# Optimization experiments

Measured on AMD Instinct MI355X. Metric: run time of the kernel, lower is better.

Reference implementation:

```python
import jax, jax.numpy as jnp
import numpy as np

EPS = 1e-5
B, S, D = 4, 2048, 128
BALL_SCALE = 0.05  # keeps points inside the unit Poincare ball for c=1


def setup_inputs() -> dict:
    key = jax.random.key(0)
    kq, kk, kv = jax.random.split(key, 3)
    q = jax.random.normal(kq, (B, S, D), dtype=jnp.float32) * BALL_SCALE
    k = jax.random.normal(kk, (B, S, D), dtype=jnp.float32) * BALL_SCALE
    v_tangent = jax.random.normal(kv, (B, S, D), dtype=jnp.float32)
    c = jnp.asarray(1.0, dtype=jnp.float32)
    beta = jnp.asarray(0.0, dtype=jnp.float32)            # nn.Parameter init 0.0
    attention_bias = jnp.asarray(0.0, dtype=jnp.float32)  # nn.Parameter init 0.0
    return {"q": q, "k": k, "v_tangent": v_tangent, "c": c,
            "beta": beta, "attention_bias": attention_bias}


def reference(q, k, v_tangent, c, beta, attention_bias):
    sqrt_c = jnp.sqrt(c)

    # --- pairwise Poincare distance (all fp32, as in the torch autocast block) ---
    x_norm_sq = jnp.sum(q * q, axis=-1, keepdims=True)            # (B,S,1)
    y_norm_sq = jnp.sum(k * k, axis=-1, keepdims=True)            # (B,S,1)
    xy_dot = jnp.einsum('bsd,btd->bst', q, k)                     # (B,S,S)
    y_norm_sq_t = jnp.swapaxes(y_norm_sq, -2, -1)                 # (B,1,S)
    diff_norm_sq = x_norm_sq - 2.0 * xy_dot + y_norm_sq_t         # ||x-y||^2, (B,S,S)
    denom = (1.0 - c * x_norm_sq) * (1.0 - c * y_norm_sq_t)       # (B,S,S)
    arg = 1.0 + 2.0 * c * diff_norm_sq / jnp.maximum(denom, EPS)
    dist = jnp.arccosh(jnp.maximum(arg, 1.0 + EPS)) / sqrt_c      # (B,S,S)

    # --- attention ---
    beta_positive = jax.nn.softplus(beta)
    attention_scores = -beta_positive * dist - attention_bias
    attention_weights = jax.nn.softmax(attention_scores, axis=-1)  # (B,S,S)
    output_tangent = jnp.einsum('bst,btd->bsd', attention_weights, v_tangent)

    # --- exp map at origin ---
    v_norm = jnp.maximum(
        jnp.sqrt(jnp.sum(output_tangent * output_tangent, axis=-1, keepdims=True)), EPS)
    output_hyperbolic = (jnp.tanh(sqrt_c * v_norm) / sqrt_c) * (output_tangent / v_norm)

    return output_hyperbolic, attention_weights
```

## Files before the change

### kernel.cpp

```cpp
#include <hip/hip_runtime.h>
#include <math.h>

#define B_ 4
#define S_ 2048
#define D_ 128
#define EPSF 1e-5f
#define BN 128
#define BN2 64
#define PSB 272

typedef __attribute__((ext_vector_type(8))) short short8;
typedef __attribute__((ext_vector_type(4))) float f32x4;

static __device__ __forceinline__ unsigned short f2bf(float f) {
    unsigned u = __float_as_uint(f);
    return (unsigned short)((u + 0x7fffu + ((u >> 16) & 1u)) >> 16);
}

static __device__ __forceinline__ void gload_lds16(const void* g, void* l) {
    __builtin_amdgcn_global_load_lds((const __attribute__((address_space(1))) unsigned*)g,
                                     (__attribute__((address_space(3))) unsigned*)l, 16, 0, 0);
}


__global__ __launch_bounds__(256) void convqk_kernel(const float* __restrict__ q,
                                                     const float* __restrict__ k,
                                                     const float* __restrict__ cp,
                                                     float* __restrict__ qn, float* __restrict__ kn,
                                                     float* __restrict__ lws,
                                                     float2* __restrict__ qng, float2* __restrict__ kng,
                                                     unsigned* __restrict__ Qb, unsigned* __restrict__ Kb) {
    int row = blockIdx.x * 4 + (threadIdx.x >> 6);
    int lane = threadIdx.x & 63;
    const int NR = B_ * S_;
    const float cc = cp[0];
    bool isQ = row < NR;
    int r = isQ ? row : row - NR;
    float2 v = ((const float2*)(isQ ? q : k))[(size_t)r * 64 + lane];
    unsigned pk = (unsigned)f2bf(v.x) | ((unsigned)f2bf(v.y) << 16);
    float nrm = v.x * v.x + v.y * v.y;
#pragma unroll
    for (int m = 1; m <= 32; m <<= 1) nrm += __shfl_xor(nrm, m, 64);
    if (isQ) {
        Qb[(size_t)r * 64 + lane] = pk;
        if (lane == 0) {
            qn[r] = nrm;
            qng[r] = make_float2(nrm, 2.f * cc * __builtin_amdgcn_rcpf(1.f - cc * nrm));
        }
        if (lane == 1) lws[r] = 0.f;
    } else {
        int c = lane >> 2;
        int cs = c ^ (r & 7);
        Kb[(size_t)r * 64 + cs * 4 + (lane & 3)] = pk;
        if (lane == 0) {
            kn[r] = nrm;
            kng[r] = make_float2(nrm, __builtin_amdgcn_rcpf(1.f - cc * nrm));
        }
    }
}

__global__ __launch_bounds__(256) void convv_kernel(const float* __restrict__ v, uint4* __restrict__ Vtb) {
    __shared__ unsigned short Vs[128 * 132];
    int b = blockIdx.x >> 4;
    int t = blockIdx.x & 15;
    int tid = threadIdx.x;
    const float* src = v + ((size_t)b * S_ + t * 128) * D_;
    int d4 = tid & 31, key0 = tid >> 5;
#pragma unroll
    for (int it = 0; it < 16; ++it) {
        int key = key0 + it * 8;
        float4 f = *(const float4*)(src + (size_t)key * D_ + d4 * 4);
        unsigned short* dst = &Vs[key * 132 + d4 * 4];
        dst[0] = f2bf(f.x); dst[1] = f2bf(f.y); dst[2] = f2bf(f.z); dst[3] = f2bf(f.w);
    }
    __syncthreads();
    uint4* tile = Vtb + (size_t)blockIdx.x * (128 * 16);
    int d = tid & 127;
    int cl = tid >> 7;
#pragma unroll
    for (int it = 0; it < 8; ++it) {
        int c = cl + it * 2;
        int kb = c * 8;
        unsigned short e0 = Vs[(kb + 0) * 132 + d], e1 = Vs[(kb + 1) * 132 + d];
        unsigned short e2 = Vs[(kb + 2) * 132 + d], e3 = Vs[(kb + 3) * 132 + d];
        unsigned short e4 = Vs[(kb + 4) * 132 + d], e5 = Vs[(kb + 5) * 132 + d];
        unsigned short e6 = Vs[(kb + 6) * 132 + d], e7 = Vs[(kb + 7) * 132 + d];
        uint4 o;
        o.x = (unsigned)e0 | ((unsigned)e1 << 16);
        o.y = (unsigned)e2 | ((unsigned)e3 << 16);
        o.z = (unsigned)e4 | ((unsigned)e5 << 16);
        o.w = (unsigned)e6 | ((unsigned)e7 << 16);
        tile[d * 16 + (c ^ (d & 7))] = o;
    }
}


__global__ __launch_bounds__(512, 2) void hattn3_kernel(
    const unsigned short* __restrict__ Qb, const char* __restrict__ Kb, const char* __restrict__ Vtb,
    const float2* __restrict__ qng, const float2* __restrict__ kng,
    const float* __restrict__ cp, const float* __restrict__ betap, const float* __restrict__ biasp,
    float* __restrict__ lws, float* __restrict__ Opart, uint4* __restrict__ Pws) {

    __shared__ __align__(1024) char smem[75648];
    char* PsB = smem + 65536;
    float* l_row = (float*)(smem + 75520);

    const int tid = threadIdx.x;
    const int lane = tid & 63, wave = tid >> 6;
    const int wm = wave & 1, wn = wave >> 1;
    const int lm = lane & 15, quad = lane >> 4;

    const int th = blockIdx.x & 1;
    const int b = (blockIdx.x >> 1) & 3;
    const int rb = blockIdx.x >> 3;
    const int s0 = rb * 32;
    const size_t bS = (size_t)b * S_;
    const int g0 = th * 16;

    const float beta = betap[0], bias = biasp[0];
    const float cc = cp[0];
    const float beta_pos = fmaxf(beta, 0.f) + log1pf(__expf(-fabsf(beta)));
    const float sqrt_c = sqrtf(cc);
    const float bneg = -beta_pos / sqrt_c;
    const float bias2 = -bias * 1.442695040888963f;
    const float onepe = 1.f + EPSF;

    const char* KbBase = Kb + bS * 256;
    const char* VtBase = Vtb + (size_t)b * 16 * 32768;

    {
        const char* ks = KbBase + (size_t)g0 * 16384;
        const char* vs = VtBase + (size_t)(g0 >> 1) * 32768 + (size_t)(g0 & 1) * 128;
#pragma unroll
        for (int j = 0; j < 2; ++j) {
            int m = tid + j * 512;
            gload_lds16(ks + m * 16, smem + m * 16);
            gload_lds16(vs + (m >> 3) * 256 + (m & 7) * 16, smem + 32768 + m * 16);
        }
        if (tid < 64) {
            float2 y = kng[bS + (size_t)g0 * 64 + tid];
            *(float2*)(smem + 74240 + tid * 8) = y;
        }
        if (tid >= 64 && tid < 96) {
            float2 x = qng[bS + s0 + (tid - 64)];
            *(float2*)(smem + 75264 + (tid - 64) * 8) = x;
        }
        if (tid >= 96 && tid < 128) l_row[tid - 96] = 0.f;
    }

    short8 aq[4];
    {
        const unsigned short* qrow = Qb + (bS + s0 + wm * 16 + lm) * D_;
#pragma unroll
        for (int ks = 0; ks < 4; ++ks)
            aq[ks] = *(const short8*)(qrow + ks * 32 + quad * 8);
    }

    f32x4 o0 = {0.f, 0.f, 0.f, 0.f}, o1 = {0.f, 0.f, 0.f, 0.f};
    float lacc[4] = {0.f, 0.f, 0.f, 0.f};

    __syncthreads();

    int p = 0;
    const int n0 = wn * 16 + lm;
    for (int it = 0; it < 16; ++it) {
        char* KsC = smem + p * 16384;
        char* VtC = smem + 32768 + p * 16384;
        const char* YGC = smem + 74240 + p * 512;

        float2 ygn;
        if (it < 15) {
            int g = g0 + it + 1;
            const char* ks = KbBase + (size_t)g * 16384;
            char* kd = smem + (p ^ 1) * 16384;
#pragma unroll
            for (int j = 0; j < 2; ++j) {
                int off = (tid + j * 512) * 16;
                gload_lds16(ks + off, kd + off);
            }
            if (tid < 64) ygn = kng[bS + (size_t)g * 64 + tid];
        }

        f32x4 acc = {0.f, 0.f, 0.f, 0.f};
#pragma unroll
        for (int ks = 0; ks < 4; ++ks) {
            int c = ks * 4 + quad;
            short8 bk = *(const short8*)(KsC + n0 * 256 + ((c ^ (n0 & 7)) * 16));
            acc = __builtin_amdgcn_mfma_f32_16x16x32_bf16(aq[ks], bk, acc, 0, 0, 0);
        }

        {
            float2 yg = *(const float2*)(YGC + n0 * 8);
#pragma unroll
            for (int r = 0; r < 4; ++r) {
                int row = wm * 16 + quad * 4 + r;
                float2 xr = *(const float2*)(smem + 75264 + row * 8);
                float diff = fmaf(-2.f, acc[r], xr.x + yg.x);
                float arg = fmaf(diff * yg.y, xr.y, 1.f);
                arg = fmaxf(arg, onepe);
                float w = arg + sqrtf(fmaf(arg, arg, -1.f));
                float pv = __builtin_amdgcn_exp2f(fmaf(bneg, __builtin_amdgcn_logf(w), bias2));
                *(unsigned short*)(PsB + row * PSB + n0 * 2) = f2bf(pv);
                lacc[r] += pv;
            }
        }
        __syncthreads();

        if (it < 15) {
            int g = g0 + it + 1;
            const char* vs = VtBase + (size_t)(g >> 1) * 32768 + (size_t)(g & 1) * 128;
            char* vd = smem + 32768 + (p ^ 1) * 16384;
#pragma unroll
            for (int j = 0; j < 2; ++j) {
                int m = tid + j * 512;
                gload_lds16(vs + (m >> 3) * 256 + (m & 7) * 16, vd + m * 16);
            }
            if (tid < 64) *(float2*)(smem + 74240 + (p ^ 1) * 512 + tid * 8) = ygn;
        }

        if (tid < 256) {
            int row = tid >> 3, ch = tid & 7;
            uint4 pv = *(const uint4*)(PsB + row * PSB + ch * 16);
            Pws[(((bS + s0 + row) * S_ + (size_t)(g0 + it) * 64) >> 3) + ch] = pv;
        }

#pragma unroll
        for (int ks2 = 0; ks2 < 2; ++ks2) {
            short8 ap = *(const short8*)(PsB + (wm * 16 + lm) * PSB + (ks2 * 32 + quad * 8) * 2);
            int d0 = wn * 32 + lm;
            int lo = ks2 * 4 + quad;
            short8 v0 = *(const short8*)(VtC + d0 * 128 + ((lo ^ (d0 & 7)) * 16));
            int d1 = d0 + 16;
            short8 v1 = *(const short8*)(VtC + d1 * 128 + ((lo ^ (d1 & 7)) * 16));
            o0 = __builtin_amdgcn_mfma_f32_16x16x32_bf16(ap, v0, o0, 0, 0, 0);
            o1 = __builtin_amdgcn_mfma_f32_16x16x32_bf16(ap, v1, o1, 0, 0, 0);
        }
        __syncthreads();
        p ^= 1;
    }

#pragma unroll
    for (int r = 0; r < 4; ++r) {
        float s = lacc[r];
#pragma unroll
        for (int m = 1; m <= 8; m <<= 1) s += __shfl_xor(s, m, 64);
        if (lm == 0) atomicAdd(&l_row[wm * 16 + quad * 4 + r], s);
    }
    __syncthreads();

    float* op = Opart + (size_t)th * (B_ * S_ * D_) + (bS + s0) * D_;
#pragma unroll
    for (int r = 0; r < 4; ++r) {
        int row = wm * 16 + quad * 4 + r;
        op[(size_t)row * D_ + wn * 32 + lm] = o0[r];
        op[(size_t)row * D_ + wn * 32 + 16 + lm] = o1[r];
    }
    if (tid < 32) atomicAdd(&lws[bS + s0 + tid], l_row[tid]);
}

__global__ __launch_bounds__(256) void hepi_kernel(const float* __restrict__ Opart,
                                                   const float* __restrict__ lws,
                                                   const float* __restrict__ cp,
                                                   float* __restrict__ hout) {
    int row = blockIdx.x * 4 + (threadIdx.x >> 6);
    int lane = threadIdx.x & 63;
    const float cc = cp[0];
    const float sqrt_c = sqrtf(cc);
    float2 a = ((const float2*)(Opart + (size_t)row * D_))[lane];
    float2 b = ((const float2*)(Opart + (size_t)(B_ * S_ * D_) + (size_t)row * D_))[lane];
    float linv = 1.f / lws[row];
    float x0 = (a.x + b.x) * linv;
    float x1 = (a.y + b.y) * linv;
    float np = x0 * x0 + x1 * x1;
#pragma unroll
    for (int m = 1; m <= 32; m <<= 1) np += __shfl_xor(np, m, 64);
    float vn = fmaxf(sqrtf(np), EPSF);
    float aa = sqrt_c * vn;
    float t = 1.f - 2.f / (__expf(2.f * aa) + 1.f);
    float sc = t / aa;
    float2 o = {x0 * sc, x1 * sc};
    ((float2*)(hout + (size_t)row * D_))[lane] = o;
}

__global__ __launch_bounds__(256) void wnorm2_kernel(const uint4* __restrict__ Pws,
                                                     const float* __restrict__ lws,
                                                     float* __restrict__ w) {
    size_t idx = (size_t)blockIdx.x * 256 + threadIdx.x;
    int row = (int)(idx >> 8);
    float linv = 1.f / lws[row];
    uint4 u = Pws[idx];
    float4 f0, f1;
    f0.x = __uint_as_float(u.x << 16) * linv;
    f0.y = __uint_as_float(u.x & 0xffff0000u) * linv;
    f0.z = __uint_as_float(u.y << 16) * linv;
    f0.w = __uint_as_float(u.y & 0xffff0000u) * linv;
    f1.x = __uint_as_float(u.z << 16) * linv;
    f1.y = __uint_as_float(u.z & 0xffff0000u) * linv;
    f1.z = __uint_as_float(u.w << 16) * linv;
    f1.w = __uint_as_float(u.w & 0xffff0000u) * linv;
    float4* out = (float4*)w + idx * 2;
    out[0] = f0;
    out[1] = f1;
}


__global__ __launch_bounds__(512, 2) void hattn_kernel(
    const unsigned short* __restrict__ Qb, const char* __restrict__ Kb, const char* __restrict__ Vtb,
    const float* __restrict__ qn, const float* __restrict__ kn,
    const float* __restrict__ cp, const float* __restrict__ betap, const float* __restrict__ biasp,
    float* __restrict__ lws, float* __restrict__ houtg, float* __restrict__ woutg) {

    __shared__ __align__(1024) char smem[75136];
    char* KsB = smem;
    char* VtB = smem + 32768;
    char* PsB = smem + 65536;
    float* kn_s  = (float*)(smem + 74240);
    float* qn_s  = (float*)(smem + 74752);
    float* l_row = (float*)(smem + 74880);
    float* nsq_s = (float*)(smem + 75008);

    const int tid = threadIdx.x;
    const int lane = tid & 63, wave = tid >> 6;
    const int wm = wave & 1, wn = wave >> 1;
    const int lm = lane & 15, quad = lane >> 4;

    int xcd = blockIdx.x & 7;
    int b = xcd >> 1;
    int rb = (blockIdx.x >> 3) * 2 + (xcd & 1);
    int s0 = rb * 32;
    const size_t bS = (size_t)b * S_;

    const float cc = cp[0], beta = betap[0], bias = biasp[0];
    const float beta_pos = fmaxf(beta, 0.f) + log1pf(__expf(-fabsf(beta)));
    const float sqrt_c = sqrtf(cc);
    const float inv_sqrt_c = 1.f / sqrt_c;

    if (tid < 32) {
        qn_s[tid] = qn[bS + s0 + tid];
        l_row[tid] = 0.f;
        nsq_s[tid] = 0.f;
    }

    short8 aq[4];
    {
        const unsigned short* qrow = Qb + (bS + s0 + wm * 16 + lm) * D_;
#pragma unroll
        for (int ks = 0; ks < 4; ++ks)
            aq[ks] = *(const short8*)(qrow + ks * 32 + quad * 8);
    }

    f32x4 o0 = {0.f, 0.f, 0.f, 0.f}, o1 = {0.f, 0.f, 0.f, 0.f};

    const char* KbBase = Kb + bS * 256;
    const char* VtBase = Vtb + (size_t)b * 16 * 32768;

    for (int t = 0; t < S_ / BN; ++t) {
        int t0 = t * BN;
        __syncthreads();
        {
            const uint4* ksrc = (const uint4*)(KbBase + (size_t)t0 * 256);
            const uint4* vsrc = (const uint4*)(VtBase + (size_t)t * 32768);
            uint4* kd = (uint4*)KsB;
            uint4* vd = (uint4*)VtB;
#pragma unroll
            for (int i = 0; i < 4; ++i) {
                kd[tid + i * 512] = ksrc[tid + i * 512];
                vd[tid + i * 512] = vsrc[tid + i * 512];
            }
            if (tid < BN) kn_s[tid] = kn[bS + t0 + tid];
        }
        __syncthreads();

        f32x4 acc0 = {0.f, 0.f, 0.f, 0.f}, acc1 = {0.f, 0.f, 0.f, 0.f};
#pragma unroll
        for (int ks = 0; ks < 4; ++ks) {
            int n0 = wn * 32 + lm;
            int c = ks * 4 + quad;
            short8 b0 = *(const short8*)(KsB + n0 * 256 + ((c ^ (n0 & 7)) * 16));
            int n1 = n0 + 16;
            short8 b1 = *(const short8*)(KsB + n1 * 256 + ((c ^ (n1 & 7)) * 16));
            acc0 = __builtin_amdgcn_mfma_f32_16x16x32_bf16(aq[ks], b0, acc0, 0, 0, 0);
            acc1 = __builtin_amdgcn_mfma_f32_16x16x32_bf16(aq[ks], b1, acc1, 0, 0, 0);
        }

        float lp[4];
#pragma unroll
        for (int r = 0; r < 4; ++r) {
            int row = wm * 16 + quad * 4 + r;
            float xn = qn_s[row];
            float fx = 1.f - cc * xn;
            float p0, p1;
#pragma unroll
            for (int nt = 0; nt < 2; ++nt) {
                int col = wn * 32 + nt * 16 + lm;
                float dot = (nt == 0) ? acc0[r] : acc1[r];
                float yn = kn_s[col];
                float diff = xn - 2.f * dot + yn;
                float den = fmaxf(fx * (1.f - cc * yn), EPSF);
                float arg = fmaf(2.f * cc * diff, __builtin_amdgcn_rcpf(den), 1.f);
                arg = fmaxf(arg, 1.f + EPSF);
                float dist = __logf(arg + sqrtf(arg * arg - 1.f)) * inv_sqrt_c;
                float p = __expf(fmaf(-beta_pos, dist, -bias));
                woutg[(bS + s0 + row) * S_ + t0 + col] = p;
                *(unsigned short*)(PsB + row * PSB + col * 2) = f2bf(p);
                if (nt == 0) p0 = p; else p1 = p;
            }
            lp[r] = p0 + p1;
        }
#pragma unroll
        for (int r = 0; r < 4; ++r) {
            float s = lp[r];
#pragma unroll
            for (int m = 1; m <= 8; m <<= 1) s += __shfl_xor(s, m, 64);
            if (lm == 0) atomicAdd(&l_row[wm * 16 + quad * 4 + r], s);
        }
        __syncthreads();

#pragma unroll
        for (int ks = 0; ks < 4; ++ks) {
            short8 ap = *(const short8*)(PsB + (wm * 16 + lm) * PSB + (ks * 32 + quad * 8) * 2);
            int d0 = wn * 32 + lm;
            int c = ks * 4 + quad;
            short8 v0 = *(const short8*)(VtB + d0 * 256 + ((c ^ (d0 & 7)) * 16));
            int d1 = d0 + 16;
            short8 v1 = *(const short8*)(VtB + d1 * 256 + ((c ^ (d1 & 7)) * 16));
            o0 = __builtin_amdgcn_mfma_f32_16x16x32_bf16(ap, v0, o0, 0, 0, 0);
            o1 = __builtin_amdgcn_mfma_f32_16x16x32_bf16(ap, v1, o1, 0, 0, 0);
        }
    }
    __syncthreads();

    float xs0[4], xs1[4];
#pragma unroll
    for (int r = 0; r < 4; ++r) {
        int row = wm * 16 + quad * 4 + r;
        float linv = __builtin_amdgcn_rcpf(l_row[row]);
        float x0 = o0[r] * linv, x1 = o1[r] * linv;
        xs0[r] = x0; xs1[r] = x1;
        float np = x0 * x0 + x1 * x1;
#pragma unroll
        for (int m = 1; m <= 8; m <<= 1) np += __shfl_xor(np, m, 64);
        if (lm == 0) atomicAdd(&nsq_s[row], np);
    }
    if (tid < 32) lws[bS + s0 + tid] = l_row[tid];
    __syncthreads();
#pragma unroll
    for (int r = 0; r < 4; ++r) {
        int row = wm * 16 + quad * 4 + r;
        float vn = fmaxf(sqrtf(nsq_s[row]), EPSF);
        float a = sqrt_c * vn;
        float th = 1.f - 2.f * __builtin_amdgcn_rcpf(__expf(2.f * a) + 1.f);
        float sc = th / a;
        houtg[(bS + s0 + row) * D_ + wn * 32 + lm] = xs0[r] * sc;
        houtg[(bS + s0 + row) * D_ + wn * 32 + 16 + lm] = xs1[r] * sc;
    }
}

__global__ __launch_bounds__(256) void wnorm_kernel(float* __restrict__ w,
                                                    const float* __restrict__ lws) {
    size_t idx = (size_t)blockIdx.x * 256 + threadIdx.x;
    int row = (int)(idx >> 9);
    float linv = 1.f / lws[row];
    float4* p = (float4*)w + idx;
    float4 v = *p;
    v.x *= linv; v.y *= linv; v.z *= linv; v.w *= linv;
    *p = v;
}


extern "C" void kernel_launch(void* const* d_in, const int* in_sizes, int n_in,
                              void* d_out, int out_size, void* d_ws, size_t ws_size,
                              hipStream_t stream) {
    const float* q    = (const float*)d_in[0];
    const float* k    = (const float*)d_in[1];
    const float* v    = (const float*)d_in[2];
    const float* c    = (const float*)d_in[3];
    const float* beta = (const float*)d_in[4];
    const float* ab   = (const float*)d_in[5];

    float* out  = (float*)d_out;
    float* hout = out;
    float* wout = out + (size_t)B_ * S_ * D_;

    float* qn  = (float*)d_ws;
    float* kn  = qn + B_ * S_;
    float* lws = kn + B_ * S_;
    char*  wsb = (char*)d_ws;
    const size_t QG_OFF = 98304;
    const size_t KG_OFF = QG_OFF + 65536;
    const size_t QB_OFF = KG_OFF + 65536;
    const size_t KB_OFF = QB_OFF + 2097152;
    const size_t VT_OFF = KB_OFF + 2097152;
    const size_t NEED1  = VT_OFF + 2097152;
    const size_t OP_OFF = NEED1;
    const size_t PW_OFF = OP_OFF + 2u * B_ * S_ * D_ * 4;
    const size_t NEED2  = PW_OFF + (size_t)B_ * S_ * S_ * 2;

    float2*  qng = (float2*)(wsb + QG_OFF);
    float2*  kng = (float2*)(wsb + KG_OFF);
    unsigned* Qb = (unsigned*)(wsb + QB_OFF);
    unsigned* Kb = (unsigned*)(wsb + KB_OFF);
    uint4*   Vtb = (uint4*)(wsb + VT_OFF);

    if (ws_size >= NEED2) {
        float* Opart = (float*)(wsb + OP_OFF);
        uint4* Pws   = (uint4*)(wsb + PW_OFF);
        convqk_kernel<<<4096, 256, 0, stream>>>(q, k, c, qn, kn, lws, qng, kng, Qb, Kb);
        convv_kernel<<<64, 256, 0, stream>>>(v, Vtb);
        hattn3_kernel<<<512, 512, 0, stream>>>((const unsigned short*)Qb, (const char*)Kb,
                                               (const char*)Vtb, qng, kng, c, beta, ab,
                                               lws, Opart, Pws);
        hepi_kernel<<<2048, 256, 0, stream>>>(Opart, lws, c, hout);
        wnorm2_kernel<<<8192, 256, 0, stream>>>(Pws, lws, wout);
    } else {
        convqk_kernel<<<4096, 256, 0, stream>>>(q, k, c, qn, kn, lws, qng, kng, Qb, Kb);
        convv_kernel<<<64, 256, 0, stream>>>(v, Vtb);
        hattn_kernel<<<256, 512, 0, stream>>>((const unsigned short*)Qb, (const char*)Kb,
                                              (const char*)Vtb, qn, kn, c, beta, ab,
                                              lws, hout, wout);
        wnorm_kernel<<<(B_ * S_ * S_ / 4) / 256, 256, 0, stream>>>(wout, lws);
    }
}
```

Measured before the change: 141.5 us.

## Fuse attention, normalization and exp-map epilogue into single full-row kernel

Replaces the split-key attention kernel plus separate epilogue and weight-normalization kernels with one 1024-thread kernel. Each block now covers a full 2048-key row range, so no partial outputs or bf16 probability workspace are needed. Unnormalized probabilities are kept in registers and written as normalized fp32 after the row sums are known, and the tanh exp-map is applied in place. This removes two kernel launches and a round trip of a large intermediate through global memory. In exchange it uses very large LDS per block, fewer blocks (256), a big register array, and strided scalar stores to the weights output.

```diff
diff --git a/kernel.cpp b/kernel.cpp
--- a/kernel.cpp
+++ b/kernel.cpp
@@ -6,7 +6,6 @@
 #define D_ 128
 #define EPSF 1e-5f
 #define BN 128
-#define BN2 64
 #define PSB 272
 
 typedef __attribute__((ext_vector_type(8))) short short8;
@@ -95,27 +94,27 @@
 }
 
 
-__global__ __launch_bounds__(512, 2) void hattn3_kernel(
+__global__ __launch_bounds__(1024, 4) void hattn4_kernel(
     const unsigned short* __restrict__ Qb, const char* __restrict__ Kb, const char* __restrict__ Vtb,
     const float2* __restrict__ qng, const float2* __restrict__ kng,
     const float* __restrict__ cp, const float* __restrict__ betap, const float* __restrict__ biasp,
-    float* __restrict__ lws, float* __restrict__ Opart, uint4* __restrict__ Pws) {
-
-    __shared__ __align__(1024) char smem[75648];
-    char* PsB = smem + 65536;
-    float* l_row = (float*)(smem + 75520);
+    float* __restrict__ hout, float* __restrict__ wout) {
+
+    __shared__ __align__(1024) char smem[142336];
+    char* PsB = smem + 131072;
+    float* l_row = (float*)(smem + 142080);
+    float* nsq_s = (float*)(smem + 142208);
 
     const int tid = threadIdx.x;
     const int lane = tid & 63, wave = tid >> 6;
     const int wm = wave & 1, wn = wave >> 1;
     const int lm = lane & 15, quad = lane >> 4;
 
-    const int th = blockIdx.x & 1;
-    const int b = (blockIdx.x >> 1) & 3;
-    const int rb = blockIdx.x >> 3;
-    const int s0 = rb * 32;
+    int xcd = blockIdx.x & 7;
+    int b = xcd >> 1;
+    int rb = (blockIdx.x >> 3) * 2 + (xcd & 1);
+    int s0 = rb * 32;
     const size_t bS = (size_t)b * S_;
-    const int g0 = th * 16;
 
     const float beta = betap[0], bias = biasp[0];
     const float cc = cp[0];
@@ -129,23 +128,23 @@
     const char* VtBase = Vtb + (size_t)b * 16 * 32768;
 
     {
-        const char* ks = KbBase + (size_t)g0 * 16384;
-        const char* vs = VtBase + (size_t)(g0 >> 1) * 32768 + (size_t)(g0 & 1) * 128;
 #pragma unroll
         for (int j = 0; j < 2; ++j) {
-            int m = tid + j * 512;
-            gload_lds16(ks + m * 16, smem + m * 16);
-            gload_lds16(vs + (m >> 3) * 256 + (m & 7) * 16, smem + 32768 + m * 16);
-        }
-        if (tid < 64) {
-            float2 y = kng[bS + (size_t)g0 * 64 + tid];
-            *(float2*)(smem + 74240 + tid * 8) = y;
-        }
-        if (tid >= 64 && tid < 96) {
-            float2 x = qng[bS + s0 + (tid - 64)];
-            *(float2*)(smem + 75264 + (tid - 64) * 8) = x;
-        }
-        if (tid >= 96 && tid < 128) l_row[tid - 96] = 0.f;
+            int m = tid + j * 1024;
+            gload_lds16(KbBase + m * 16, smem + m * 16);
+            gload_lds16(VtBase + m * 16, smem + 65536 + m * 16);
+        }
+        if (tid < 128) {
+            float2 y = kng[bS + tid];
+            *(float2*)(smem + 139776 + tid * 8) = y;
+        } else if (tid < 160) {
+            float2 x = qng[bS + s0 + (tid - 128)];
+            *(float2*)(smem + 141824 + (tid - 128) * 8) = x;
+        } else if (tid < 192) {
+            l_row[tid - 160] = 0.f;
+        } else if (tid < 224) {
+            nsq_s[tid - 192] = 0.f;
+        }
     }
 
     short8 aq[4];
@@ -156,29 +155,33 @@
             aq[ks] = *(const short8*)(qrow + ks * 32 + quad * 8);
     }
 
-    f32x4 o0 = {0.f, 0.f, 0.f, 0.f}, o1 = {0.f, 0.f, 0.f, 0.f};
+    f32x4 o = {0.f, 0.f, 0.f, 0.f};
     float lacc[4] = {0.f, 0.f, 0.f, 0.f};
+    unsigned pst[32];
 
     __syncthreads();
 
     int p = 0;
     const int n0 = wn * 16 + lm;
+#pragma unroll
     for (int it = 0; it < 16; ++it) {
-        char* KsC = smem + p * 16384;
-        char* VtC = smem + 32768 + p * 16384;
-        const char* YGC = smem + 74240 + p * 512;
+        char* KsC = smem + p * 32768;
+        char* VtC = smem + 65536 + p * 32768;
+        const char* YGC = smem + 139776 + p * 1024;
 
         float2 ygn;
         if (it < 15) {
-            int g = g0 + it + 1;
-            const char* ks = KbBase + (size_t)g * 16384;
-            char* kd = smem + (p ^ 1) * 16384;
+            const char* ks = KbBase + (size_t)(it + 1) * 32768;
+            const char* vs = VtBase + (size_t)(it + 1) * 32768;
+            char* kd = smem + (p ^ 1) * 32768;
+            char* vd = smem + 65536 + (p ^ 1) * 32768;
 #pragma unroll
             for (int j = 0; j < 2; ++j) {
-                int off = (tid + j * 512) * 16;
+                int off = (tid + j * 1024) * 16;
                 gload_lds16(ks + off, kd + off);
+                gload_lds16(vs + off, vd + off);
             }
-            if (tid < 64) ygn = kng[bS + (size_t)g * 64 + tid];
+            if (tid < 128) ygn = kng[bS + (size_t)(it + 1) * 128 + tid];
         }
 
         f32x4 acc = {0.f, 0.f, 0.f, 0.f};
@@ -191,49 +194,37 @@
 
         {
             float2 yg = *(const float2*)(YGC + n0 * 8);
+            unsigned pw0 = 0, pw1 = 0;
 #pragma unroll
             for (int r = 0; r < 4; ++r) {
                 int row = wm * 16 + quad * 4 + r;
-                float2 xr = *(const float2*)(smem + 75264 + row * 8);
+                float2 xr = *(const float2*)(smem + 141824 + row * 8);
                 float diff = fmaf(-2.f, acc[r], xr.x + yg.x);
                 float arg = fmaf(diff * yg.y, xr.y, 1.f);
                 arg = fmaxf(arg, onepe);
                 float w = arg + sqrtf(fmaf(arg, arg, -1.f));
                 float pv = __builtin_amdgcn_exp2f(fmaf(bneg, __builtin_amdgcn_logf(w), bias2));
-                *(unsigned short*)(PsB + row * PSB + n0 * 2) = f2bf(pv);
+                unsigned short pb = f2bf(pv);
+                *(unsigned short*)(PsB + row * PSB + n0 * 2) = pb;
                 lacc[r] += pv;
+                if (r == 0) pw0 = pb;
+                else if (r == 1) pw0 |= (unsigned)pb << 16;
+                else if (r == 2) pw1 = pb;
+                else pw1 |= (unsigned)pb << 16;
             }
+            pst[it * 2] = pw0;
+            pst[it * 2 + 1] = pw1;
         }
         __syncthreads();
 
-        if (it < 15) {
-            int g = g0 + it + 1;
-            const char* vs = VtBase + (size_t)(g >> 1) * 32768 + (size_t)(g & 1) * 128;
-            char* vd = smem + 32768 + (p ^ 1) * 16384;
-#pragma unroll
-            for (int j = 0; j < 2; ++j) {
-                int m = tid + j * 512;
-                gload_lds16(vs + (m >> 3) * 256 + (m & 7) * 16, vd + m * 16);
-            }
-            if (tid < 64) *(float2*)(smem + 74240 + (p ^ 1) * 512 + tid * 8) = ygn;
-        }
-
-        if (tid < 256) {
-            int row = tid >> 3, ch = tid & 7;
-            uint4 pv = *(const uint4*)(PsB + row * PSB + ch * 16);
-            Pws[(((bS + s0 + row) * S_ + (size_t)(g0 + it) * 64) >> 3) + ch] = pv;
-        }
-
-#pragma unroll
-        for (int ks2 = 0; ks2 < 2; ++ks2) {
-            short8 ap = *(const short8*)(PsB + (wm * 16 + lm) * PSB + (ks2 * 32 + quad * 8) * 2);
-            int d0 = wn * 32 + lm;
-            int lo = ks2 * 4 + quad;
-            short8 v0 = *(const short8*)(VtC + d0 * 128 + ((lo ^ (d0 & 7)) * 16));
-            int d1 = d0 + 16;
-            short8 v1 = *(const short8*)(VtC + d1 * 128 + ((lo ^ (d1 & 7)) * 16));
-            o0 = __builtin_amdgcn_mfma_f32_16x16x32_bf16(ap, v0, o0, 0, 0, 0);
-            o1 = __builtin_amdgcn_mfma_f32_16x16x32_bf16(ap, v1, o1, 0, 0, 0);
+        if (it < 15 && tid < 128) *(float2*)(smem + 139776 + (p ^ 1) * 1024 + tid * 8) = ygn;
+
+#pragma unroll
+        for (int ks = 0; ks < 4; ++ks) {
+            short8 ap = *(const short8*)(PsB + (wm * 16 + lm) * PSB + (ks * 32 + quad * 8) * 2);
+            int c = ks * 4 + quad;
+            short8 vv = *(const short8*)(VtC + n0 * 256 + ((c ^ (n0 & 7)) * 16));
+            o = __builtin_amdgcn_mfma_f32_16x16x32_bf16(ap, vv, o, 0, 0, 0);
         }
         __syncthreads();
         p ^= 1;
@@ -248,59 +239,47 @@
     }
     __syncthreads();
 
-    float* op = Opart + (size_t)th * (B_ * S_ * D_) + (bS + s0) * D_;
+    float linv[4];
+#pragma unroll
+    for (int r = 0; r < 4; ++r) linv[r] = 1.f / l_row[wm * 16 + quad * 4 + r];
+
+#pragma unroll
+    for (int r = 0; r < 4; ++r) {
+        float x = o[r] * linv[r];
+        o[r] = x;
+        float np = x * x;
+#pragma unroll
+        for (int m = 1; m <= 8; m <<= 1) np += __shfl_xor(np, m, 64);
+        if (lm == 0) atomicAdd(&nsq_s[wm * 16 + quad * 4 + r], np);
+    }
+    __syncthreads();
 #pragma unroll
     for (int r = 0; r < 4; ++r) {
         int row = wm * 16 + quad * 4 + r;
-        op[(size_t)row * D_ + wn * 32 + lm] = o0[r];
-        op[(size_t)row * D_ + wn * 32 + 16 + lm] = o1[r];
-    }
-    if (tid < 32) atomicAdd(&lws[bS + s0 + tid], l_row[tid]);
-}
-
-__global__ __launch_bounds__(256) void hepi_kernel(const float* __restrict__ Opart,
-                                                   const float* __restrict__ lws,
-                                                   const float* __restrict__ cp,
-                                                   float* __restrict__ hout) {
-    int row = blockIdx.x * 4 + (threadIdx.x >> 6);
-    int lane = threadIdx.x & 63;
-    const float cc = cp[0];
-    const float sqrt_c = sqrtf(cc);
-    float2 a = ((const float2*)(Opart + (size_t)row * D_))[lane];
-    float2 b = ((const float2*)(Opart + (size_t)(B_ * S_ * D_) + (size_t)row * D_))[lane];
-    float linv = 1.f / lws[row];
-    float x0 = (a.x + b.x) * linv;
-    float x1 = (a.y + b.y) * linv;
-    float np = x0 * x0 + x1 * x1;
-#pragma unroll
-    for (int m = 1; m <= 32; m <<= 1) np += __shfl_xor(np, m, 64);
-    float vn = fmaxf(sqrtf(np), EPSF);
-    float aa = sqrt_c * vn;
-    float t = 1.f - 2.f / (__expf(2.f * aa) + 1.f);
-    float sc = t / aa;
-    float2 o = {x0 * sc, x1 * sc};
-    ((float2*)(hout + (size_t)row * D_))[lane] = o;
-}
-
-__global__ __launch_bounds__(256) void wnorm2_kernel(const uint4* __restrict__ Pws,
-                                                     const float* __restrict__ lws,
-                                                     float* __restrict__ w) {
-    size_t idx = (size_t)blockIdx.x * 256 + threadIdx.x;
-    int row = (int)(idx >> 8);
-    float linv = 1.f / lws[row];
-    uint4 u = Pws[idx];
-    float4 f0, f1;
-    f0.x = __uint_as_float(u.x << 16) * linv;
-    f0.y = __uint_as_float(u.x & 0xffff0000u) * linv;
-    f0.z = __uint_as_float(u.y << 16) * linv;
-    f0.w = __uint_as_float(u.y & 0xffff0000u) * linv;
-    f1.x = __uint_as_float(u.z << 16) * linv;
-    f1.y = __uint_as_float(u.z & 0xffff0000u) * linv;
-    f1.z = __uint_as_float(u.w << 16) * linv;
-    f1.w = __uint_as_float(u.w & 0xffff0000u) * linv;
-    float4* out = (float4*)w + idx * 2;
-    out[0] = f0;
-    out[1] = f1;
+        float vn = fmaxf(sqrtf(nsq_s[row]), EPSF);
+        float a = sqrt_c * vn;
+        float th = 1.f - 2.f / (__expf(2.f * a) + 1.f);
+        float sc = th / a;
+        hout[(bS + s0 + row) * D_ + n0] = o[r] * sc;
+    }
+
+    {
+        const size_t wbase = (bS + s0) * (size_t)S_;
+        const int row0 = wm * 16 + quad * 4;
+#pragma unroll
+        for (int it = 0; it < 16; ++it) {
+            unsigned pw0 = pst[it * 2], pw1 = pst[it * 2 + 1];
+            float p0 = __uint_as_float(pw0 << 16) * linv[0];
+            float p1 = __uint_as_float(pw0 & 0xffff0000u) * linv[1];
+            float p2 = __uint_as_float(pw1 << 16) * linv[2];
+            float p3 = __uint_as_float(pw1 & 0xffff0000u) * linv[3];
+            size_t cg = wbase + (size_t)it * 128 + n0;
+            wout[cg + (size_t)(row0 + 0) * S_] = p0;
+            wout[cg + (size_t)(row0 + 1) * S_] = p1;
+            wout[cg + (size_t)(row0 + 2) * S_] = p2;
+            wout[cg + (size_t)(row0 + 3) * S_] = p3;
+        }
+    }
 }
 
 
@@ -492,9 +471,6 @@
     const size_t KB_OFF = QB_OFF + 2097152;
     const size_t VT_OFF = KB_OFF + 2097152;
     const size_t NEED1  = VT_OFF + 2097152;
-    const size_t OP_OFF = NEED1;
-    const size_t PW_OFF = OP_OFF + 2u * B_ * S_ * D_ * 4;
-    const size_t NEED2  = PW_OFF + (size_t)B_ * S_ * S_ * 2;
 
     float2*  qng = (float2*)(wsb + QG_OFF);
     float2*  kng = (float2*)(wsb + KG_OFF);
@@ -502,16 +478,12 @@
     unsigned* Kb = (unsigned*)(wsb + KB_OFF);
     uint4*   Vtb = (uint4*)(wsb + VT_OFF);
 
-    if (ws_size >= NEED2) {
-        float* Opart = (float*)(wsb + OP_OFF);
-        uint4* Pws   = (uint4*)(wsb + PW_OFF);
+    if (ws_size >= NEED1) {
         convqk_kernel<<<4096, 256, 0, stream>>>(q, k, c, qn, kn, lws, qng, kng, Qb, Kb);
         convv_kernel<<<64, 256, 0, stream>>>(v, Vtb);
-        hattn3_kernel<<<512, 512, 0, stream>>>((const unsigned short*)Qb, (const char*)Kb,
-                                               (const char*)Vtb, qng, kng, c, beta, ab,
-                                               lws, Opart, Pws);
-        hepi_kernel<<<2048, 256, 0, stream>>>(Opart, lws, c, hout);
-        wnorm2_kernel<<<8192, 256, 0, stream>>>(Pws, lws, wout);
+        hattn4_kernel<<<256, 1024, 0, stream>>>((const unsigned short*)Qb, (const char*)Kb,
+                                                (const char*)Vtb, qng, kng, c, beta, ab,
+                                                hout, wout);
     } else {
         convqk_kernel<<<4096, 256, 0, stream>>>(q, k, c, qn, kn, lws, qng, kng, Qb, Kb);
         convv_kernel<<<64, 256, 0, stream>>>(v, Vtb);
```

After: 150.3 us. 6.2% more time.
